# Kernel tuning notes

Measured on AMD Instinct MI355X. Metric: run time of the kernel, lower is better.

## Reference

```python
import jax, jax.numpy as jnp
import numpy as np

B, N, HID = 1, 2048, 2048
NH, NKV, HD = 16, 4, 128
GROUPS = NH // NKV
CHUNK = 64          # get_valid_chunk_size(B*NH*N=32768, 64) == 64
MAG = 0.5
GATE_NORM = 16.0


def setup_inputs() -> dict:
    key = jax.random.key(0)
    ks = jax.random.split(key, 5)
    s = 0.02
    return {
        "hidden_states": jax.random.normal(ks[0], (B, N, HID), jnp.float32),
        "Wq": jax.random.normal(ks[1], (NH * HD, HID), jnp.float32) * s,
        "Wk": jax.random.normal(ks[2], (NKV * HD, HID), jnp.float32) * s,
        "Wv": jax.random.normal(ks[3], (NKV * HD, HID), jnp.float32) * s,
        "Wo": jax.random.normal(ks[4], (HID, NH * HD), jnp.float32) * s,
    }


def _delta_rule_chunked(q, k, v, beta, chunk_size):
    """Chunkwise delta-rule linear attention (DeltaNet chunk form).
    q,k,v,beta: [T, d] flattened tokens; returns (o [T,d], final_state [d,d])."""
    T, d = q.shape
    n = T // chunk_size
    qc, kc, vc, bc = (x.reshape(n, chunk_size, d) for x in (q, k, v, beta))
    kb = kc * bc                       # beta-weighted keys
    vb = vc * bc                       # beta-weighted values
    strict = jnp.tril(jnp.ones((chunk_size, chunk_size), bool), -1)
    eye = jnp.eye(chunk_size, dtype=q.dtype)
    # A = I + strictly-lower(k_beta k^T); unit lower triangular -> invert by triangular solve
    A = eye + jnp.where(strict, jnp.einsum('ncd,nkd->nck', kb, kc), 0.0)
    Tinv = jax.vmap(lambda a: jax.scipy.linalg.solve_triangular(a, eye, lower=True))(A)
    w = Tinv @ kb                      # [n, C, d]
    u = Tinv @ vb                      # [n, C, d]
    causal = jnp.tril(jnp.ones((chunk_size, chunk_size), bool))

    def step(S, inp):
        qi, ki, wi, ui = inp           # each [C, d]
        u_i = ui - wi @ S              # correct pseudo-values by inter-chunk state
        attn = jnp.where(causal, qi @ ki.T, 0.0)
        o = qi @ S + attn @ u_i
        return S + ki.T @ u_i, o

    S0 = jnp.zeros((d, d), q.dtype)
    Sf, o = jax.lax.scan(step, S0, (qc, kc, w, u))
    return o.reshape(T, d), Sf


def _forward(hidden_states, Wq, Wk, Wv, Wo):
    q = hidden_states @ Wq.T           # [B, N, NH*HD]
    k = hidden_states @ Wk.T           # [B, N, NKV*HD]
    v = hidden_states @ Wv.T           # [B, N, NKV*HD]
    g = k                              # AdaptiveAvgPool1d(512 -> 512) is identity
    qh = q.reshape(B, N, NH, HD).transpose(0, 2, 1, 3)   # b h n d
    kh = k.reshape(B, N, NKV, HD).transpose(0, 2, 1, 3)
    vh = v.reshape(B, N, NKV, HD).transpose(0, 2, 1, 3)
    gh = g.reshape(B, N, NKV, HD).transpose(0, 2, 1, 3)
    rep = lambda x: jnp.repeat(x, GROUPS, axis=1)        # repeat_kv
    khr, vhr, ghr = rep(kh), rep(vh), rep(gh)

    # linear-attention path: softmax feature maps + logsigmoid gate
    ql = jax.nn.softmax(qh, axis=-1).astype(jnp.float32)
    kl = jax.nn.softmax(khr, axis=-1).astype(jnp.float32)
    gl = (jax.nn.log_sigmoid(ghr) / GATE_NORM).astype(jnp.float32)
    vl = vhr.astype(jnp.float32)
    flat = lambda x: x.reshape(B * NH * N, HD)
    o_lin, _ = _delta_rule_chunked(flat(ql), flat(kl), flat(vl), flat(gl), CHUNK)
    o_lin = o_lin.reshape(B, NH, N, HD).transpose(0, 2, 1, 3).reshape(B, N, NH * HD)
    o_lin = o_lin @ Wo.T

    # base (vanilla causal softmax) attention path
    scores = jnp.einsum('bhnd,bhmd->bhnm', qh, khr) * (HD ** -0.5)
    cmask = jnp.tril(jnp.ones((N, N), bool))
    scores = jnp.where(cmask[None, None], scores, jnp.finfo(scores.dtype).min)
    attn = jax.nn.softmax(scores, axis=-1)
    o_base = jnp.einsum('bhnm,bhmd->bhnd', attn, vhr)
    o_base = o_base.transpose(0, 2, 1, 3).reshape(B, N, NH * HD) @ Wo.T

    return MAG * o_lin + (1.0 - MAG) * o_base


def reference(hidden_states, Wq, Wk, Wv, Wo):
    return _forward(hidden_states, Wq, Wk, Wv, Wo)
```

## Files before the change

kernel.cpp:

```cpp
#include <hip/hip_runtime.h>
#include <hip/hip_bf16.h>

typedef unsigned short u16;
typedef unsigned int u32;
typedef __bf16 bf16x8 __attribute__((ext_vector_type(8)));
typedef float f32x4 __attribute__((ext_vector_type(4)));

#define MFMA16(a,b,c) __builtin_amdgcn_mfma_f32_16x16x32_bf16((a),(b),(c),0,0,0)

__device__ __forceinline__ u16 f2bf(float f){
  u32 u = __builtin_bit_cast(u32, f);
  u32 r = (u + 0x7fffu + ((u >> 16) & 1u)) >> 16;
  return (u16)r;
}
__device__ __forceinline__ float bf2f(u16 h){
  u32 u = ((u32)h) << 16;
  return __builtin_bit_cast(float, u);
}
__device__ __forceinline__ void splitbf(float x, u16& hi, u16& lo){
  hi = f2bf(x);
  lo = f2bf(x - bf2f(hi));
}
__device__ __forceinline__ void gload_lds16(const u16* g, u16* l){
  __builtin_amdgcn_global_load_lds((__attribute__((address_space(1))) void*)(g),
                                   (__attribute__((address_space(3))) void*)(l), 16, 0, 0);
}
__device__ __forceinline__ const u16* selu(const u16* barr, const u16* parr, int i){
  return (i < 128) ? (barr + (size_t)i*16384) : (parr + (size_t)(i-128)*16384);
}
__device__ __forceinline__ const float* self32(const float* barr, const float* parr, int i){
  return (i < 128) ? (barr + (size_t)i*16384) : (parr + (size_t)(i-128)*16384);
}
__device__ __forceinline__ float* slotp(float* p1, float* p2, int s){
  return (s < 381) ? (p1 + (size_t)s*16512) : (p2 + (size_t)(s-381)*16512);
}
__device__ __forceinline__ const float* slotpc(const float* p1, const float* p2, int s){
  return (s < 381) ? (p1 + (size_t)s*16512) : (p2 + (size_t)(s-381)*16512);
}
__device__ __forceinline__ float* tdq(float* Td, int row, int colc){
  return Td + row*132 + ((colc ^ ((row >> 3) & 7)) << 2);
}

constexpr size_t OF_HSBF   = 0;
constexpr size_t OF_WQKVBF = 8388608;
constexpr size_t OF_WOBF   = 20971520;
constexpr size_t OF_QKV    = 29360128;
constexpr size_t OF_QBF    = 54525952;
constexpr size_t OF_KBF    = 62914560;
constexpr size_t OF_VT     = 65011712;
constexpr size_t OF_QLB    = 67108864;
constexpr size_t OF_KLF    = 75497472;
constexpr size_t OF_KLB    = 79691776;
constexpr size_t OF_GLF    = 81788928;
constexpr size_t OF_TINV   = 85983232;
constexpr size_t OF_WF     = 88080384;
constexpr size_t OF_WB     = 92274688;
constexpr size_t OF_U0     = 94371840;
constexpr size_t OF_SJ     = 111149056;
constexpr size_t OF_OMIX   = 127926272;
constexpr size_t OF_OMIXB  = 144703488;
constexpr size_t OF_ADF  = 102760448;
constexpr size_t OF_ABTF = OF_OMIX;
constexpr size_t OF_ADH  = OF_OMIX + 8388608;
constexpr size_t OF_ADL  = OF_OMIX + 12582912;
constexpr size_t OF_ADTH = OF_OMIXB;
constexpr size_t OF_ADTL = OF_OMIXB + 4194304;
constexpr size_t OF_ABTH = OF_KLF;
constexpr size_t OF_ABTL = OF_GLF;
constexpr size_t OF_BDF  = OF_QKV;
constexpr size_t OF_BBTF = OF_QKV + 8388608;
constexpr size_t OF_BDH  = OF_QKV + 16777216;
constexpr size_t OF_BDL  = OF_QKV + 20971520;
constexpr size_t OF_BDTH = OF_HSBF;
constexpr size_t OF_BDTL = OF_HSBF + 4194304;
constexpr size_t OF_BBTH = OF_WQKVBF;
constexpr size_t OF_BBTL = OF_WQKVBF + 4194304;
constexpr size_t OF_TTF  = OF_TINV;
constexpr size_t OF_TTH  = OF_WQKVBF + 8388608;
constexpr size_t OF_TTL  = OF_WQKVBF + 8912896;
constexpr size_t OF_PDF  = OF_ADF;
constexpr size_t OF_PBTF = OF_ADF + 1048576;
constexpr size_t OF_PDH  = OF_ADF + 2097152;
constexpr size_t OF_PDL  = OF_ADF + 2621440;
constexpr size_t OF_PDTH = OF_ADF + 3145728;
constexpr size_t OF_PDTL = OF_ADF + 3670016;
constexpr size_t OF_PBTH = OF_ADF + 4194304;
constexpr size_t OF_PBTL = OF_ADF + 4718592;
constexpr size_t OF_APART1 = OF_QKV;
constexpr size_t OF_APART2 = OF_OMIXB;
constexpr size_t OF_OBF = 0;

struct CompJobs { int a[8]; int b[8]; int d[8]; };

__global__ void k_f2ball(const float* __restrict__ hs, const float* __restrict__ Wq,
                         const float* __restrict__ Wk, const float* __restrict__ Wv,
                         const float* __restrict__ Wo, u16* __restrict__ hs_bf,
                         u16* __restrict__ wqkv_bf, u16* __restrict__ wo_bf){
  int bid = blockIdx.x;
  const float* src; u16* dst; int off;
  if(bid < 4096){ src = hs; dst = hs_bf; off = bid; }
  else if(bid < 8192){ src = Wq; dst = wqkv_bf; off = bid - 4096; }
  else if(bid < 9216){ src = Wk; dst = wqkv_bf + 2048*2048; off = bid - 8192; }
  else if(bid < 10240){ src = Wv; dst = wqkv_bf + 2560*2048; off = bid - 9216; }
  else { src = Wo; dst = wo_bf; off = bid - 10240; }
  int i = (off*256 + threadIdx.x) * 4;
  f32x4 v = *(const f32x4*)(src + i);
  u32 w0 = (u32)f2bf(v[0]) | ((u32)f2bf(v[1]) << 16);
  u32 w1 = (u32)f2bf(v[2]) | ((u32)f2bf(v[3]) << 16);
  *(u32*)(dst + i) = w0;
  *(u32*)(dst + i + 2) = w1;
}

__global__ __launch_bounds__(256) void k_gemm(const u16* __restrict__ A, const u16* __restrict__ B,
                                              float* __restrict__ C, int K, int N){
  __shared__ u16 aL[128*32];
  __shared__ u16 bL[128*32];
  int lin = blockIdx.y * gridDim.x + blockIdx.x;
  int nwg = gridDim.x * gridDim.y;
  int s = (lin & 7) * (nwg >> 3) + (lin >> 3);
  int bn = s % gridDim.x, bm = s / gridDim.x;
  int tid = threadIdx.x, lane = tid & 63, w = tid >> 6;
  int wm = w >> 1, wn = w & 1;
  f32x4 acc[4][4] = {};
  int nK = K >> 5;
  const u16* Abase = A + (size_t)bm * 128 * K;
  const u16* Bbase = B + (size_t)bn * 128 * K;
  for(int kt = 0; kt < nK; ++kt){
    __syncthreads();
    #pragma unroll
    for(int t = 0; t < 2; ++t){
      int row = t*64 + w*16 + (lane >> 2);
      int kc = (lane & 3) * 8;
      gload_lds16(Abase + (size_t)row*K + kt*32 + kc, &aL[(t*64 + w*16)*32]);
      gload_lds16(Bbase + (size_t)row*K + kt*32 + kc, &bL[(t*64 + w*16)*32]);
    }
    __syncthreads();
    bf16x8 af[4], bf[4];
    #pragma unroll
    for(int i = 0; i < 4; ++i){
      af[i] = *(const bf16x8*)&aL[(wm*64 + i*16 + (lane & 15))*32 + ((lane >> 4) << 3)];
      bf[i] = *(const bf16x8*)&bL[(wn*64 + i*16 + (lane & 15))*32 + ((lane >> 4) << 3)];
    }
    #pragma unroll
    for(int i = 0; i < 4; ++i)
      #pragma unroll
      for(int j = 0; j < 4; ++j)
        acc[i][j] = MFMA16(af[i], bf[j], acc[i][j]);
  }
  #pragma unroll
  for(int i = 0; i < 4; ++i)
    #pragma unroll
    for(int j = 0; j < 4; ++j)
      #pragma unroll
      for(int r = 0; r < 4; ++r){
        int row = bm*128 + wm*64 + i*16 + ((lane >> 4) << 2) + r;
        int col = bn*128 + wn*64 + j*16 + (lane & 15);
        C[(size_t)row * N + col] = acc[i][j][r];
      }
}

__global__ __launch_bounds__(256) void k_linvt(const float* __restrict__ qkv, u16* qbf, u16* qlb,
                                               u16* kbf, float* klf, u16* klb, float* glf,
                                               u16* __restrict__ vT){
  __shared__ float t[64][65];
  int bid = blockIdx.x;
  if(bid < 10240){
    int gtask = bid * 4 + (threadIdx.x >> 6);
    int lane = threadIdx.x & 63;
    int n = gtask / 20, tt = gtask % 20;
    const float* row = (tt < 16) ? (qkv + (size_t)n*3072 + tt*128)
                                 : (qkv + (size_t)n*3072 + 2048 + (tt-16)*128);
    float v0 = row[lane], v1 = row[lane + 64];
    float m = fmaxf(v0, v1);
    #pragma unroll
    for(int o = 1; o < 64; o <<= 1) m = fmaxf(m, __shfl_xor(m, o, 64));
    float e0 = __expf(v0 - m), e1 = __expf(v1 - m);
    float s = e0 + e1;
    #pragma unroll
    for(int o = 1; o < 64; o <<= 1) s += __shfl_xor(s, o, 64);
    float r0 = e0 / s, r1 = e1 / s;
    if(tt < 16){
      size_t base = ((size_t)tt*2048 + n) * 128;
      qbf[base + lane] = f2bf(v0); qbf[base + 64 + lane] = f2bf(v1);
      qlb[base + lane] = f2bf(r0); qlb[base + 64 + lane] = f2bf(r1);
    } else {
      int g = tt - 16;
      size_t base = ((size_t)g*2048 + n) * 128;
      kbf[base + lane] = f2bf(v0); kbf[base + 64 + lane] = f2bf(v1);
      klf[base + lane] = r0;       klf[base + 64 + lane] = r1;
      klb[base + lane] = f2bf(r0); klb[base + 64 + lane] = f2bf(r1);
      float g0 = (fminf(v0, 0.f) - log1pf(__expf(-fabsf(v0)))) * (1.f/16.f);
      float g1 = (fminf(v1, 0.f) - log1pf(__expf(-fabsf(v1)))) * (1.f/16.f);
      glf[base + lane] = g0; glf[base + 64 + lane] = g1;
    }
  } else {
    int v = bid - 10240;
    int nt = v & 31, dt = (v >> 5) & 1, g = v >> 6;
    int tid = threadIdx.x;
    {
      int r = tid >> 2, c0 = (tid & 3) * 16;
      const float* src = qkv + (size_t)(nt*64 + r)*3072 + 2560 + g*128 + dt*64 + c0;
      #pragma unroll
      for(int q = 0; q < 16; q += 4){
        f32x4 vv = *(const f32x4*)(src + q);
        t[r][c0+q] = vv[0]; t[r][c0+q+1] = vv[1]; t[r][c0+q+2] = vv[2]; t[r][c0+q+3] = vv[3];
      }
    }
    __syncthreads();
    {
      int d = tid >> 2, c0 = (tid & 3) * 16;
      u16* dst = vT + ((size_t)g*128 + dt*64 + d)*2048 + (size_t)nt*64 + c0;
      #pragma unroll
      for(int half = 0; half < 2; ++half){
        int b = c0 + half*8;
        u32 w0 = (u32)f2bf(t[b+0][d]) | ((u32)f2bf(t[b+1][d]) << 16);
        u32 w1 = (u32)f2bf(t[b+2][d]) | ((u32)f2bf(t[b+3][d]) << 16);
        u32 w2 = (u32)f2bf(t[b+4][d]) | ((u32)f2bf(t[b+5][d]) << 16);
        u32 w3 = (u32)f2bf(t[b+6][d]) | ((u32)f2bf(t[b+7][d]) << 16);
        *(uint4*)(dst + half*8) = make_uint4(w0, w1, w2, w3);
      }
    }
  }
}

__global__ __launch_bounds__(256) void k_prep1(const float* __restrict__ klf, const float* __restrict__ glf,
                                               float* __restrict__ tinv){
  __shared__ float KlT[128][68];
  __shared__ float Kb[64][132];
  __shared__ float Am[64][68];
  __shared__ float XT[64][68];
  int idx = blockIdx.x, g = idx >> 5, c = idx & 31, tid = threadIdx.x;
  size_t base = ((size_t)g*2048 + c*64) * 128;
  {
    int r = tid >> 2, d0 = (tid & 3) * 32;
    #pragma unroll
    for(int dd = 0; dd < 32; dd += 4){
      f32x4 kv = *(const f32x4*)(klf + base + r*128 + d0 + dd);
      f32x4 gv = *(const f32x4*)(glf + base + r*128 + d0 + dd);
      KlT[d0+dd][r] = kv[0]; KlT[d0+dd+1][r] = kv[1]; KlT[d0+dd+2][r] = kv[2]; KlT[d0+dd+3][r] = kv[3];
      f32x4 kb = kv * gv;
      *(f32x4*)&Kb[r][d0+dd] = kb;
    }
  }
  __syncthreads();
  {
    int i = tid >> 2, j0 = (tid & 3) * 16;
    f32x4 s[4] = {};
    for(int d = 0; d < 128; ++d){
      float kb = Kb[i][d];
      #pragma unroll
      for(int q = 0; q < 4; ++q){
        f32x4 kl = *(const f32x4*)&KlT[d][j0 + q*4];
        s[q] += kb * kl;
      }
    }
    #pragma unroll
    for(int q = 0; q < 4; ++q) *(f32x4*)&Am[i][j0 + q*4] = s[q];
  }
  __syncthreads();
  if(tid < 64){
    int cc = tid;
    float x0 = (cc == 0) ? 1.f : 0.f;
    XT[cc][0] = x0;
    tinv[(size_t)idx*4096 + cc] = x0;
    for(int i = 1; i < 64; ++i){
      float s = (i == cc) ? 1.f : 0.f;
      int i4 = i & ~3;
      for(int jj = 0; jj < i4; jj += 4){
        f32x4 av = *(const f32x4*)&Am[i][jj];
        f32x4 xv = *(const f32x4*)&XT[cc][jj];
        s -= av[0]*xv[0] + av[1]*xv[1] + av[2]*xv[2] + av[3]*xv[3];
      }
      for(int jj = i4; jj < i; ++jj) s -= Am[i][jj] * XT[cc][jj];
      XT[cc][i] = s;
      tinv[(size_t)idx*4096 + i*64 + cc] = s;
    }
  }
}

__global__ __launch_bounds__(256) void k_prep2a(const float* __restrict__ klf, const float* __restrict__ glf,
                                                const float* __restrict__ qkv, const float* __restrict__ tinv,
                                                float* __restrict__ wf, u16* __restrict__ wb, float* __restrict__ u0f){
  __shared__ char smem[51200];
  float (*Ti)[68] = (float(*)[68])smem;
  float (*B)[132] = (float(*)[132])(smem + 17408);
  int bid = blockIdx.x, idx = bid >> 1, z = bid & 1;
  int g = idx >> 5, c = idx & 31, tid = threadIdx.x;
  size_t base = ((size_t)g*2048 + c*64) * 128;
  {
    int r = tid >> 2, d0 = (tid & 3) * 32;
    #pragma unroll
    for(int dd = 0; dd < 32; dd += 4){
      f32x4 gv = *(const f32x4*)(glf + base + r*128 + d0 + dd);
      f32x4 xv;
      if(z == 0) xv = *(const f32x4*)(klf + base + r*128 + d0 + dd);
      else       xv = *(const f32x4*)(qkv + (size_t)(c*64 + r)*3072 + 2560 + g*128 + d0 + dd);
      *(f32x4*)&B[r][d0+dd] = xv * gv;
    }
    int c0 = (tid & 3) * 16;
    #pragma unroll
    for(int q = 0; q < 16; q += 4)
      *(f32x4*)&Ti[r][c0+q] = *(const f32x4*)(tinv + (size_t)idx*4096 + r*64 + c0 + q);
  }
  __syncthreads();
  int i = tid >> 2, cc0 = (tid & 3) * 32;
  f32x4 wa[8] = {};
  for(int jj = 0; jj < 64; ++jj){
    float a = Ti[i][jj];
    #pragma unroll
    for(int q = 0; q < 8; ++q)
      wa[q] += a * *(const f32x4*)&B[jj][cc0 + q*4];
  }
  __syncthreads();
  float (*Tw)[132] = (float(*)[132])smem;
  #pragma unroll
  for(int q = 0; q < 8; ++q)
    *(f32x4*)&Tw[i][cc0 + q*4] = wa[q];
  __syncthreads();
  size_t ob = (size_t)idx * 8192;
  #pragma unroll
  for(int c2 = 0; c2 < 8; ++c2){
    int ii = c2*1024 + tid*4;
    int row = ii >> 7, col = ii & 127;
    f32x4 wv = *(const f32x4*)&Tw[row][col];
    if(z == 0){
      *(f32x4*)(wf + ob + ii) = wv;
      u32 p0 = (u32)f2bf(wv[0]) | ((u32)f2bf(wv[1]) << 16);
      u32 p1 = (u32)f2bf(wv[2]) | ((u32)f2bf(wv[3]) << 16);
      *(u32*)(wb + ob + ii) = p0;
      *(u32*)(wb + ob + ii + 2) = p1;
    } else {
      *(f32x4*)(u0f + ob + ii) = wv;
    }
  }
}

__global__ __launch_bounds__(256) void k_prep2b(const float* __restrict__ klf, const float* __restrict__ wf,
                                                const float* __restrict__ u0f,
                                                float* __restrict__ dF, u16* __restrict__ dH, u16* __restrict__ dL,
                                                u16* __restrict__ dTH, u16* __restrict__ dTL,
                                                float* __restrict__ btF, u16* __restrict__ btH, u16* __restrict__ btL){
  __shared__ char smem[67584];
  float (*Kl)[132] = (float(*)[132])smem;
  float (*Wm)[132] = (float(*)[132])(smem + 33792);
  int bid = blockIdx.x, idx = bid >> 1, z = bid & 1;
  int g = idx >> 5, c = idx & 31, tid = threadIdx.x;
  size_t base = ((size_t)g*2048 + c*64) * 128;
  {
    int r = tid >> 2, d0 = (tid & 3) * 32;
    const float* src = (z == 0) ? wf : u0f;
    #pragma unroll
    for(int dd = 0; dd < 32; dd += 4){
      *(f32x4*)&Kl[r][d0+dd] = *(const f32x4*)(klf + base + r*128 + d0 + dd);
      *(f32x4*)&Wm[r][d0+dd] = *(const f32x4*)(src + (size_t)idx*8192 + r*128 + d0 + dd);
    }
  }
  __syncthreads();
  int a = tid >> 1, b0 = (tid & 1) * 64;
  f32x4 pa[16] = {};
  if(z == 0){
    for(int r = 0; r < 64; ++r){
      float ka = Kl[r][a];
      #pragma unroll
      for(int q = 0; q < 16; ++q)
        pa[q] += ka * *(const f32x4*)&Wm[r][b0 + q*4];
    }
    #pragma unroll
    for(int q = 0; q < 16; ++q) pa[q] = -pa[q];
  } else {
    for(int r = 0; r < 64; ++r){
      float ua = Wm[r][a];
      #pragma unroll
      for(int q = 0; q < 16; ++q)
        pa[q] += ua * *(const f32x4*)&Kl[r][b0 + q*4];
    }
  }
  __syncthreads();
  float* Td = (float*)smem;
  #pragma unroll
  for(int q = 0; q < 16; ++q)
    *(f32x4*)tdq(Td, a, (b0 >> 2) + q) = pa[q];
  __syncthreads();
  size_t ob = (size_t)idx * 16384;
  if(z == 0){
    #pragma unroll
    for(int c2 = 0; c2 < 16; ++c2){
      int ii = c2*1024 + tid*4;
      int row = ii >> 7, col = ii & 127;
      f32x4 dv = *(const f32x4*)tdq(Td, row, col >> 2);
      *(f32x4*)(dF + ob + ii) = dv;
      u16 h0,l0,h1,l1,h2,l2,h3,l3;
      splitbf(dv[0], h0, l0); splitbf(dv[1], h1, l1);
      splitbf(dv[2], h2, l2); splitbf(dv[3], h3, l3);
      *(u32*)(dH + ob + ii)     = (u32)h0 | ((u32)h1 << 16);
      *(u32*)(dH + ob + ii + 2) = (u32)h2 | ((u32)h3 << 16);
      *(u32*)(dL + ob + ii)     = (u32)l0 | ((u32)l1 << 16);
      *(u32*)(dL + ob + ii + 2) = (u32)l2 | ((u32)l3 << 16);
    }
    #pragma unroll
    for(int c2 = 0; c2 < 8; ++c2){
      int o0 = c2*2048 + tid*8;
      int b = o0 >> 7, a0 = o0 & 127;
      u16 th[8], tl[8];
      #pragma unroll
      for(int e = 0; e < 8; ++e){
        float v = *((const float*)tdq(Td, a0 + e, b >> 2) + (b & 3));
        splitbf(v, th[e], tl[e]);
      }
      uint4 ph = make_uint4((u32)th[0] | ((u32)th[1] << 16), (u32)th[2] | ((u32)th[3] << 16),
                            (u32)th[4] | ((u32)th[5] << 16), (u32)th[6] | ((u32)th[7] << 16));
      uint4 plv = make_uint4((u32)tl[0] | ((u32)tl[1] << 16), (u32)tl[2] | ((u32)tl[3] << 16),
                             (u32)tl[4] | ((u32)tl[5] << 16), (u32)tl[6] | ((u32)tl[7] << 16));
      *(uint4*)(dTH + ob + o0) = ph;
      *(uint4*)(dTL + ob + o0) = plv;
    }
  } else {
    #pragma unroll
    for(int c2 = 0; c2 < 16; ++c2){
      int ii = c2*1024 + tid*4;
      int row = ii >> 7, col = ii & 127;
      f32x4 cv = *(const f32x4*)tdq(Td, row, col >> 2);
      *(f32x4*)(btF + ob + ii) = cv;
      u16 h0,l0,h1,l1,h2,l2,h3,l3;
      splitbf(cv[0], h0, l0); splitbf(cv[1], h1, l1);
      splitbf(cv[2], h2, l2); splitbf(cv[3], h3, l3);
      *(u32*)(btH + ob + ii)     = (u32)h0 | ((u32)h1 << 16);
      *(u32*)(btH + ob + ii + 2) = (u32)h2 | ((u32)h3 << 16);
      *(u32*)(btL + ob + ii)     = (u32)l0 | ((u32)l1 << 16);
      *(u32*)(btL + ob + ii + 2) = (u32)l2 | ((u32)l3 << 16);
    }
  }
}

__global__ __launch_bounds__(256) void k_ks(
    const float* __restrict__ sDF, const u16* __restrict__ sDH, const u16* __restrict__ sDL,
    const u16* __restrict__ sDTH, const u16* __restrict__ sDTL,
    const float* __restrict__ sBF, const u16* __restrict__ sBH, const u16* __restrict__ sBL,
    float* __restrict__ dDF, u16* __restrict__ dDH, u16* __restrict__ dDL,
    u16* __restrict__ dDTH, u16* __restrict__ dDTL,
    float* __restrict__ dBF, u16* __restrict__ dBH, u16* __restrict__ dBL, int off){
  __shared__ float T[128][132];
  int c = blockIdx.x, g = blockIdx.y, z = blockIdx.z;
  int idx = g*32 + c, tid = threadIdx.x;
  size_t base = (size_t)idx * 16384;
  if(c < off){
    if(z == 0){
      for(int i = tid; i < 4096; i += 256) ((uint4*)(dDF + base))[i] = ((const uint4*)(sDF + base))[i];
      for(int i = tid; i < 2048; i += 256){
        ((uint4*)(dDH + base))[i] = ((const uint4*)(sDH + base))[i];
        ((uint4*)(dDL + base))[i] = ((const uint4*)(sDL + base))[i];
        ((uint4*)(dDTH + base))[i] = ((const uint4*)(sDTH + base))[i];
        ((uint4*)(dDTL + base))[i] = ((const uint4*)(sDTL + base))[i];
      }
    } else {
      for(int i = tid; i < 4096; i += 256) ((uint4*)(dBF + base))[i] = ((const uint4*)(sBF + base))[i];
      for(int i = tid; i < 2048; i += 256){
        ((uint4*)(dBH + base))[i] = ((const uint4*)(sBH + base))[i];
        ((uint4*)(dBL + base))[i] = ((const uint4*)(sBL + base))[i];
      }
    }
    return;
  }
  size_t blo = (size_t)(idx - off) * 16384;
  int lane = tid & 63, w = tid >> 6;
  const u16 *Ah, *Al, *Bh, *Bl;
  if(z == 0){ Ah = sDH + base; Al = sDL + base; Bh = sDTH + blo; Bl = sDTL + blo; }
  else      { Ah = sBH + blo;  Al = sBL + blo;  Bh = sDH + base; Bl = sDL + base; }
  f32x4 acc[2][8] = {};
  #pragma unroll
  for(int ks = 0; ks < 4; ++ks){
    bf16x8 ah[2], al[2], bh[8], bl[8];
    #pragma unroll
    for(int mt = 0; mt < 2; ++mt){
      int ro = (w*32 + mt*16 + (lane & 15))*128 + ks*32 + ((lane >> 4) << 3);
      ah[mt] = *(const bf16x8*)(Ah + ro);
      al[mt] = *(const bf16x8*)(Al + ro);
    }
    #pragma unroll
    for(int nt = 0; nt < 8; ++nt){
      int ro = (nt*16 + (lane & 15))*128 + ks*32 + ((lane >> 4) << 3);
      bh[nt] = *(const bf16x8*)(Bh + ro);
      bl[nt] = *(const bf16x8*)(Bl + ro);
    }
    #pragma unroll
    for(int mt = 0; mt < 2; ++mt)
      #pragma unroll
      for(int nt = 0; nt < 8; ++nt)
        acc[mt][nt] = MFMA16(ah[mt], bh[nt],
                      MFMA16(ah[mt], bl[nt],
                      MFMA16(al[mt], bh[nt], acc[mt][nt])));
  }
  if(z == 0){
    #pragma unroll
    for(int mt = 0; mt < 2; ++mt)
      #pragma unroll
      for(int nt = 0; nt < 8; ++nt)
        #pragma unroll
        for(int r = 0; r < 4; ++r){
          int row = w*32 + mt*16 + ((lane >> 4) << 2) + r;
          int col = nt*16 + (lane & 15);
          float v = acc[mt][nt][r] + sDF[base + row*128 + col] + sDF[blo + row*128 + col];
          dDF[base + row*128 + col] = v;
          u16 hi, lo; splitbf(v, hi, lo);
          dDH[base + row*128 + col] = hi;
          dDL[base + row*128 + col] = lo;
          T[row][col] = v;
        }
    __syncthreads();
    int tcol = tid >> 1, half = tid & 1;
    for(int m = 0; m < 64; ++m){
      float v = T[half*64 + m][tcol];
      u16 hi, lo; splitbf(v, hi, lo);
      dDTH[base + (size_t)tcol*128 + half*64 + m] = hi;
      dDTL[base + (size_t)tcol*128 + half*64 + m] = lo;
    }
  } else {
    #pragma unroll
    for(int mt = 0; mt < 2; ++mt)
      #pragma unroll
      for(int nt = 0; nt < 8; ++nt)
        #pragma unroll
        for(int r = 0; r < 4; ++r){
          int row = w*32 + mt*16 + ((lane >> 4) << 2) + r;
          int col = nt*16 + (lane & 15);
          float v = acc[mt][nt][r] + sBF[base + row*128 + col] + sBF[blo + row*128 + col];
          dBF[base + row*128 + col] = v;
          u16 hi, lo; splitbf(v, hi, lo);
          dBH[base + row*128 + col] = hi;
          dBL[base + row*128 + col] = lo;
        }
  }
}

__device__ __forceinline__ void comp_mfma(const u16* Ah, const u16* Al, const u16* Bh, const u16* Bl,
                                          f32x4 (&acc)[2][8], int lane, int w){
  #pragma unroll
  for(int ks = 0; ks < 4; ++ks){
    bf16x8 ah[2], al[2], bh[8], bl[8];
    #pragma unroll
    for(int mt = 0; mt < 2; ++mt){
      int ro = (w*32 + mt*16 + (lane & 15))*128 + ks*32 + ((lane >> 4) << 3);
      ah[mt] = *(const bf16x8*)(Ah + ro);
      al[mt] = *(const bf16x8*)(Al + ro);
    }
    #pragma unroll
    for(int nt = 0; nt < 8; ++nt){
      int ro = (nt*16 + (lane & 15))*128 + ks*32 + ((lane >> 4) << 3);
      bh[nt] = *(const bf16x8*)(Bh + ro);
      bl[nt] = *(const bf16x8*)(Bl + ro);
    }
    #pragma unroll
    for(int mt = 0; mt < 2; ++mt)
      #pragma unroll
      for(int nt = 0; nt < 8; ++nt)
        acc[mt][nt] = MFMA16(ah[mt], bh[nt],
                      MFMA16(ah[mt], bl[nt],
                      MFMA16(al[mt], bh[nt], acc[mt][nt])));
  }
}

__global__ __launch_bounds__(256) void k_comp(
    const float* __restrict__ bDF, const u16* __restrict__ bDH, const u16* __restrict__ bDL,
    const u16* __restrict__ bDTH, const u16* __restrict__ bDTL,
    const float* __restrict__ bBTF, const u16* __restrict__ bBTH, const u16* __restrict__ bBTL,
    float* __restrict__ pDF, u16* __restrict__ pDH, u16* __restrict__ pDL,
    u16* __restrict__ pDTH, u16* __restrict__ pDTL,
    float* __restrict__ pBTF, u16* __restrict__ pBTH, u16* __restrict__ pBTL,
    CompJobs jobs){
  __shared__ float T[128][132];
  int job = blockIdx.x, z = blockIdx.y, tid = threadIdx.x;
  int a = jobs.a[job], b = jobs.b[job], d = jobs.d[job] - 128;
  size_t ob = (size_t)d * 16384;
  int lane = tid & 63, w = tid >> 6;
  const u16 *Ah, *Al, *Bh, *Bl;
  const float *F1, *F2;
  if(z == 0){
    Ah = selu(bDH, pDH, a);  Al = selu(bDL, pDL, a);
    Bh = selu(bDTH, pDTH, b); Bl = selu(bDTL, pDTL, b);
    F1 = self32(bDF, pDF, a); F2 = self32(bDF, pDF, b);
  } else {
    Ah = selu(bBTH, pBTH, b); Al = selu(bBTL, pBTL, b);
    Bh = selu(bDH, pDH, a);   Bl = selu(bDL, pDL, a);
    F1 = self32(bBTF, pBTF, a); F2 = self32(bBTF, pBTF, b);
  }
  for(int i = tid*4; i < 16384; i += 1024){
    f32x4 v1 = *(const f32x4*)(F1 + i);
    f32x4 v2 = *(const f32x4*)(F2 + i);
    f32x4 sv = v1 + v2;
    int row = i >> 7, col = i & 127;
    *(f32x4*)&T[row][col] = sv;
  }
  __syncthreads();
  f32x4 acc[2][8] = {};
  comp_mfma(Ah, Al, Bh, Bl, acc, lane, w);
  if(z == 0){
    #pragma unroll
    for(int mt = 0; mt < 2; ++mt)
      #pragma unroll
      for(int nt = 0; nt < 8; ++nt)
        #pragma unroll
        for(int r = 0; r < 4; ++r){
          int row = w*32 + mt*16 + ((lane >> 4) << 2) + r;
          int col = nt*16 + (lane & 15);
          float v = acc[mt][nt][r] + T[row][col];
          pDF[ob + row*128 + col] = v;
          u16 hi, lo; splitbf(v, hi, lo);
          pDH[ob + row*128 + col] = hi;
          pDL[ob + row*128 + col] = lo;
          T[row][col] = v;
        }
    __syncthreads();
    int tcol = tid >> 1, half = tid & 1;
    for(int m = 0; m < 64; ++m){
      float v = T[half*64 + m][tcol];
      u16 hi, lo; splitbf(v, hi, lo);
      pDTH[ob + (size_t)tcol*128 + half*64 + m] = hi;
      pDTL[ob + (size_t)tcol*128 + half*64 + m] = lo;
    }
  } else {
    #pragma unroll
    for(int mt = 0; mt < 2; ++mt)
      #pragma unroll
      for(int nt = 0; nt < 8; ++nt)
        #pragma unroll
        for(int r = 0; r < 4; ++r){
          int row = w*32 + mt*16 + ((lane >> 4) << 2) + r;
          int col = nt*16 + (lane & 15);
          float v = acc[mt][nt][r] + T[row][col];
          pBTF[ob + row*128 + col] = v;
          u16 hi, lo; splitbf(v, hi, lo);
          pBTH[ob + row*128 + col] = hi;
          pBTL[ob + row*128 + col] = lo;
        }
  }
}

__global__ __launch_bounds__(256) void k_heads(
    const u16* __restrict__ bDH, const u16* __restrict__ bDL,
    const float* __restrict__ bBTF, const u16* __restrict__ bBTH, const u16* __restrict__ bBTL,
    const u16* __restrict__ pDH, const u16* __restrict__ pDL,
    const float* __restrict__ pBTF, const u16* __restrict__ pBTH, const u16* __restrict__ pBTL,
    float* __restrict__ ttF, u16* __restrict__ ttH, u16* __restrict__ ttL, u16* __restrict__ sj){
  __shared__ float T[128][132];
  int h = blockIdx.x, g = h >> 2, i0 = h & 3;
  int tid = threadIdx.x, lane = tid & 63, w = tid >> 6;
  int psi = (g == 0) ? -1 : (g == 1 ? 136 : (g == 2 ? 140 : 142));
  int phi = (i0 == 0) ? -1 : (i0 == 1 ? g*32 + 31 : (i0 == 2 ? 128 + g : 132 + g));
  const float* Pf = (psi >= 0) ? self32(bBTF, pBTF, psi) : nullptr;
  const float* Ff = (phi >= 0) ? self32(bBTF, pBTF, phi) : nullptr;
  for(int i = tid*4; i < 16384; i += 1024){
    f32x4 sv = {};
    if(Pf) sv += *(const f32x4*)(Pf + i);
    if(Ff) sv += *(const f32x4*)(Ff + i);
    int row = i >> 7, col = i & 127;
    *(f32x4*)&T[row][col] = sv;
  }
  __syncthreads();
  f32x4 acc[2][8] = {};
  if(psi >= 0 && phi >= 0)
    comp_mfma(selu(bBTH,pBTH,psi), selu(bBTL,pBTL,psi), selu(bDH,pDH,phi), selu(bDL,pDL,phi), acc, lane, w);
  #pragma unroll
  for(int mt = 0; mt < 2; ++mt)
    #pragma unroll
    for(int nt = 0; nt < 8; ++nt)
      #pragma unroll
      for(int r = 0; r < 4; ++r){
        int row = w*32 + mt*16 + ((lane >> 4) << 2) + r;
        int col = nt*16 + (lane & 15);
        float v = acc[mt][nt][r] + T[row][col];
        u16 hi, lo; splitbf(v, hi, lo);
        size_t o = (size_t)h*16384 + row*128 + col;
        ttF[o] = v; ttH[o] = hi; ttL[o] = lo;
        sj[(size_t)(h*32)*16384 + row*128 + col] = hi;
      }
}

__global__ __launch_bounds__(256) void k_expand(const u16* __restrict__ bDH, const u16* __restrict__ bDL,
                                                const float* __restrict__ bBF, const float* __restrict__ ttF,
                                                const u16* __restrict__ ttH, const u16* __restrict__ ttL,
                                                u16* __restrict__ sj){
  int j = blockIdx.x;
  int c = j & 31;
  if(c == 0) return;
  int h = j >> 5, g = h >> 2;
  size_t obase = (size_t)j * 16384;
  size_t mb = (size_t)(g*32 + c - 1) * 16384;
  size_t tb = (size_t)h * 16384;
  int tid = threadIdx.x, lane = tid & 63, w = tid >> 6;
  f32x4 acc[2][8] = {};
  comp_mfma(ttH + tb, ttL + tb, bDH + mb, bDL + mb, acc, lane, w);
  #pragma unroll
  for(int mt = 0; mt < 2; ++mt)
    #pragma unroll
    for(int nt = 0; nt < 8; ++nt)
      #pragma unroll
      for(int r = 0; r < 4; ++r){
        int row = w*32 + mt*16 + ((lane >> 4) << 2) + r;
        int col = nt*16 + (lane & 15);
        float v = acc[mt][nt][r] + ttF[tb + row*128 + col] + bBF[mb + row*128 + col];
        sj[obase + row*128 + col] = f2bf(v);
      }
}

__global__ __launch_bounds__(256) void k_olin(const u16* __restrict__ qlb, const u16* __restrict__ klb,
                                              const u16* __restrict__ wb, const float* __restrict__ u0f,
                                              const u16* __restrict__ sj, float* __restrict__ omix){
  __shared__ u16 ut[128*64];
  __shared__ u16 pl[4][16*64];
  int j = blockIdx.x;
  int h = j >> 5, c = j & 31, g = h >> 2, idx = g*32 + c;
  int tid = threadIdx.x, lane = tid & 63, w = tid >> 6;
  const u16* Sj = sj + (size_t)j * 16384;
  const u16* Q  = qlb + ((size_t)h*2048 + c*64) * 128;
  const u16* Kc = klb + ((size_t)g*2048 + c*64) * 128;
  const u16* W  = wb + (size_t)idx * 8192;
  const float* U0 = u0f + (size_t)idx * 8192;
  bf16x8 aq[4], aw[4];
  #pragma unroll
  for(int ks = 0; ks < 4; ++ks){
    aq[ks] = *(const bf16x8*)(Q + (w*16 + (lane & 15))*128 + ks*32 + ((lane >> 4) << 3));
    aw[ks] = *(const bf16x8*)(W + (w*16 + (lane & 15))*128 + ks*32 + ((lane >> 4) << 3));
  }
  f32x4 t1[8] = {}, ui[8] = {};
  #pragma unroll
  for(int ks = 0; ks < 4; ++ks)
    #pragma unroll
    for(int nt = 0; nt < 8; ++nt){
      bf16x8 b = *(const bf16x8*)(Sj + (nt*16 + (lane & 15))*128 + ks*32 + ((lane >> 4) << 3));
      t1[nt] = MFMA16(aq[ks], b, t1[nt]);
      ui[nt] = MFMA16(aw[ks], b, ui[nt]);
    }
  f32x4 sc[4] = {};
  #pragma unroll
  for(int ks = 0; ks < 4; ++ks)
    #pragma unroll
    for(int nt = 0; nt < 4; ++nt){
      bf16x8 b = *(const bf16x8*)(Kc + (nt*16 + (lane & 15))*128 + ks*32 + ((lane >> 4) << 3));
      sc[nt] = MFMA16(aq[ks], b, sc[nt]);
    }
  #pragma unroll
  for(int nt = 0; nt < 4; ++nt)
    #pragma unroll
    for(int r = 0; r < 4; ++r){
      int row = ((lane >> 4) << 2) + r;
      int col = nt*16 + (lane & 15);
      int grow = w*16 + row;
      float v = (col <= grow) ? sc[nt][r] : 0.f;
      int bo = (row*128 + col*2) ^ ((row & 7) << 4);
      *(u16*)((char*)&pl[w][0] + bo) = f2bf(v);
    }
  #pragma unroll
  for(int nt = 0; nt < 8; ++nt)
    #pragma unroll
    for(int r = 0; r < 4; ++r){
      int kv = w*16 + ((lane >> 4) << 2) + r;
      int d  = nt*16 + (lane & 15);
      float v = U0[kv*128 + d] - ui[nt][r];
      int bo = (d*128 + kv*2) ^ ((d & 7) << 4);
      *(u16*)((char*)ut + bo) = f2bf(v);
    }
  __syncthreads();
  f32x4 o2[8] = {};
  #pragma unroll
  for(int ks2 = 0; ks2 < 2; ++ks2){
    int row = lane & 15;
    int boA = (row*128 + ks2*64 + ((lane >> 4) << 4)) ^ ((row & 7) << 4);
    bf16x8 a = *(const bf16x8*)((const char*)&pl[w][0] + boA);
    #pragma unroll
    for(int nt = 0; nt < 8; ++nt){
      int d = nt*16 + (lane & 15);
      int boB = (d*128 + ks2*64 + ((lane >> 4) << 4)) ^ ((d & 7) << 4);
      bf16x8 b = *(const bf16x8*)((const char*)ut + boB);
      o2[nt] = MFMA16(a, b, o2[nt]);
    }
  }
  #pragma unroll
  for(int nt = 0; nt < 8; ++nt)
    #pragma unroll
    for(int r = 0; r < 4; ++r){
      int grow = c*64 + w*16 + ((lane >> 4) << 2) + r;
      int d = nt*16 + (lane & 15);
      omix[(size_t)grow*2048 + h*128 + d] = 0.5f * (t1[nt][r] + o2[nt][r]);
    }
}

__global__ __launch_bounds__(256) void k_attn(const u16* __restrict__ qbf, const u16* __restrict__ kbf,
                                              const u16* __restrict__ vT, const float* __restrict__ omix,
                                              u16* __restrict__ obf,
                                              float* __restrict__ part1, float* __restrict__ part2){
  __shared__ u16 Kl[4096];
  __shared__ u16 Vl[4096];
  __shared__ u16 pl[4][1280];
  int rb = blockIdx.x;
  int bid = (rb & 7) * 80 + (rb >> 3);
  int h = bid / 40, j = bid % 40;
  int qB, kt0, kt1, slot = -1;
  if(j < 4){ qB = j; kt0 = 0; kt1 = 4*(qB+1); }
  else {
    int jj = j - 4; int seg;
    if(jj < 8){ qB = 4 + (jj >> 1); seg = jj & 1; }
    else if(jj < 20){ int q = jj - 8; qB = 8 + q/3; seg = q - (qB-8)*3; }
    else { int q = jj - 20; qB = 12 + (q >> 2); seg = q & 3; }
    slot = h*36 + jj;
    kt0 = seg*16;
    int full = 4*(qB+1);
    kt1 = (kt0 + 16 < full) ? kt0 + 16 : full;
  }
  int g = h >> 2;
  int tid = threadIdx.x, lane = tid & 63, w = tid >> 6;
  const u16* K = kbf + (size_t)g*2048*128;
  const u16* V = vT + (size_t)g*128*2048;
  bf16x8 aq[2][4];
  #pragma unroll
  for(int m = 0; m < 2; ++m){
    const u16* Q = qbf + ((size_t)h*2048 + qB*128 + w*32 + m*16) * 128;
    #pragma unroll
    for(int ks = 0; ks < 4; ++ks)
      aq[m][ks] = *(const bf16x8*)(Q + (lane & 15)*128 + ks*32 + ((lane >> 4) << 3));
  }
  f32x4 acc[2][8] = {};
  float lsum[2][4] = {};
  const float scale = 0.08838834764831845f;
  int qr0[2];
  #pragma unroll
  for(int m = 0; m < 2; ++m) qr0[m] = qB*128 + w*32 + m*16 + ((lane >> 4) << 2);
  u16* plw = &pl[w][0];
  for(int kt = kt0; kt < kt1; ++kt){
    __syncthreads();
    #pragma unroll
    for(int inst = 0; inst < 2; ++inst){
      int ob = w*2048 + inst*1024;
      int lo = ob + lane*16;
      {
        int r = lo >> 8;
        int gc = ((lo >> 4) & 15) ^ (r & 7);
        gload_lds16(K + (size_t)(kt*32 + r)*128 + gc*8, (u16*)((char*)Kl + ob));
      }
      {
        int d = lo >> 6;
        int gnb = ((lo >> 4) & 3) ^ ((d >> 1) & 3);
        gload_lds16(V + (size_t)d*2048 + kt*32 + gnb*8, (u16*)((char*)Vl + ob));
      }
    }
    __syncthreads();
    bf16x8 kb[8];
    #pragma unroll
    for(int ct = 0; ct < 2; ++ct)
      #pragma unroll
      for(int ks = 0; ks < 4; ++ks){
        int r = ct*16 + (lane & 15);
        int pc = (ks*4 + (lane >> 4)) ^ (r & 7);
        kb[ct*4+ks] = *(const bf16x8*)(Kl + r*128 + pc*8);
      }
    f32x4 s[2][2] = {};
    #pragma unroll
    for(int m = 0; m < 2; ++m)
      #pragma unroll
      for(int ct = 0; ct < 2; ++ct)
        #pragma unroll
        for(int ks = 0; ks < 4; ++ks)
          s[m][ct] = MFMA16(aq[m][ks], kb[ct*4+ks], s[m][ct]);
    bf16x8 bv[8];
    #pragma unroll
    for(int nt = 0; nt < 8; ++nt){
      int d = nt*16 + (lane & 15);
      int pnb = (lane >> 4) ^ ((d >> 1) & 3);
      bv[nt] = *(const bf16x8*)(Vl + d*32 + pnb*8);
    }
    #pragma unroll
    for(int m = 0; m < 2; ++m)
      #pragma unroll
      for(int ct = 0; ct < 2; ++ct)
        #pragma unroll
        for(int r = 0; r < 4; ++r){
          int col = kt*32 + ct*16 + (lane & 15);
          float p = (col <= qr0[m] + r) ? __expf(s[m][ct][r] * scale) : 0.f;
          lsum[m][r] += p;
          int row = m*16 + ((lane >> 4) << 2) + r;
          *(u16*)((char*)plw + row*80 + (ct*16 + (lane & 15))*2) = f2bf(p);
        }
    __builtin_amdgcn_s_setprio(1);
    #pragma unroll
    for(int m = 0; m < 2; ++m){
      bf16x8 ap = *(const bf16x8*)((const char*)plw + (m*16 + (lane & 15))*80 + ((lane >> 4) << 4));
      #pragma unroll
      for(int nt = 0; nt < 8; ++nt)
        acc[m][nt] = MFMA16(ap, bv[nt], acc[m][nt]);
    }
    __builtin_amdgcn_s_setprio(0);
  }
  #pragma unroll
  for(int m = 0; m < 2; ++m)
    #pragma unroll
    for(int r = 0; r < 4; ++r){
      float v = lsum[m][r];
      v += __shfl_xor(v, 1, 64); v += __shfl_xor(v, 2, 64);
      v += __shfl_xor(v, 4, 64); v += __shfl_xor(v, 8, 64);
      lsum[m][r] = v;
    }
  if(slot < 0){
    #pragma unroll
    for(int m = 0; m < 2; ++m)
      #pragma unroll
      for(int nt = 0; nt < 8; ++nt)
        #pragma unroll
        for(int r = 0; r < 4; ++r){
          int row = qB*128 + w*32 + m*16 + ((lane >> 4) << 2) + r;
          int d = nt*16 + (lane & 15);
          size_t o = (size_t)row*2048 + h*128 + d;
          float fin = omix[o] + 0.5f * acc[m][nt][r] / lsum[m][r];
          obf[o] = f2bf(fin);
        }
  } else {
    float* P = slotp(part1, part2, slot);
    #pragma unroll
    for(int m = 0; m < 2; ++m)
      #pragma unroll
      for(int nt = 0; nt < 8; ++nt)
        #pragma unroll
        for(int r = 0; r < 4; ++r){
          int row = w*32 + m*16 + ((lane >> 4) << 2) + r;
          int d = nt*16 + (lane & 15);
          P[(size_t)row*128 + d] = acc[m][nt][r];
        }
    if((lane & 15) == 0)
      #pragma unroll
      for(int m = 0; m < 2; ++m)
        #pragma unroll
        for(int r = 0; r < 4; ++r)
          P[16384 + w*32 + m*16 + ((lane >> 4) << 2) + r] = lsum[m][r];
  }
}

__global__ __launch_bounds__(256) void k_acomb(const float* __restrict__ part1, const float* __restrict__ part2,
                                               const float* __restrict__ omix, u16* __restrict__ obf){
  int bid = blockIdx.x;
  int h = bid / 12, qx = bid % 12, qB = 4 + qx;
  int nseg = (qB >= 12) ? 4 : (qB >= 8) ? 3 : 2;
  int off = (qB < 8) ? (qB-4)*2 : (qB < 12) ? 8 + (qB-8)*3 : 20 + (qB-12)*4;
  int s0 = h*36 + off;
  int tid = threadIdx.x;
  #pragma unroll
  for(int it = 0; it < 16; ++it){
    int i = it*1024 + tid*4;
    int row = i >> 7;
    f32x4 a = {};
    float l = 0.f;
    for(int s = 0; s < nseg; ++s){
      const float* P = slotpc(part1, part2, s0 + s);
      a += *(const f32x4*)(P + i);
      l += P[16384 + row];
    }
    size_t idx = (size_t)(qB*128 + row)*2048 + h*128 + (i & 127);
    f32x4 cur = *(const f32x4*)(omix + idx);
    f32x4 fin = cur + a * (0.5f / l);
    u32 w0 = (u32)f2bf(fin[0]) | ((u32)f2bf(fin[1]) << 16);
    u32 w1 = (u32)f2bf(fin[2]) | ((u32)f2bf(fin[3]) << 16);
    *(u32*)(obf + idx) = w0;
    *(u32*)(obf + idx + 2) = w1;
  }
}

extern "C" void kernel_launch(void* const* d_in, const int* in_sizes, int n_in,
                              void* d_out, int out_size, void* d_ws, size_t ws_size,
                              hipStream_t stream){
  (void)in_sizes; (void)n_in; (void)out_size; (void)ws_size;
  const float* hs = (const float*)d_in[0];
  const float* Wq = (const float*)d_in[1];
  const float* Wk = (const float*)d_in[2];
  const float* Wv = (const float*)d_in[3];
  const float* Wo = (const float*)d_in[4];
  float* out = (float*)d_out;
  char* ws = (char*)d_ws;

  u16*   hs_bf   = (u16*)(ws + OF_HSBF);
  u16*   wqkv_bf = (u16*)(ws + OF_WQKVBF);
  u16*   wo_bf   = (u16*)(ws + OF_WOBF);
  float* qkv     = (float*)(ws + OF_QKV);
  u16*   qbf     = (u16*)(ws + OF_QBF);
  u16*   kbf     = (u16*)(ws + OF_KBF);
  u16*   vT      = (u16*)(ws + OF_VT);
  u16*   qlb     = (u16*)(ws + OF_QLB);
  float* klf     = (float*)(ws + OF_KLF);
  u16*   klb     = (u16*)(ws + OF_KLB);
  float* glf     = (float*)(ws + OF_GLF);
  float* tinvb   = (float*)(ws + OF_TINV);
  float* wf      = (float*)(ws + OF_WF);
  u16*   wb      = (u16*)(ws + OF_WB);
  float* u0f     = (float*)(ws + OF_U0);
  u16*   sjb     = (u16*)(ws + OF_SJ);
  float* omix    = (float*)(ws + OF_OMIX);
  u16*   obf     = (u16*)(ws + OF_OBF);
  float* aDF  = (float*)(ws + OF_ADF);
  u16*   aDH  = (u16*)(ws + OF_ADH);
  u16*   aDL  = (u16*)(ws + OF_ADL);
  u16*   aDTH = (u16*)(ws + OF_ADTH);
  u16*   aDTL = (u16*)(ws + OF_ADTL);
  float* aBTF = (float*)(ws + OF_ABTF);
  u16*   aBTH = (u16*)(ws + OF_ABTH);
  u16*   aBTL = (u16*)(ws + OF_ABTL);
  float* bDF  = (float*)(ws + OF_BDF);
  u16*   bDH  = (u16*)(ws + OF_BDH);
  u16*   bDL  = (u16*)(ws + OF_BDL);
  u16*   bDTH = (u16*)(ws + OF_BDTH);
  u16*   bDTL = (u16*)(ws + OF_BDTL);
  float* bBTF = (float*)(ws + OF_BBTF);
  u16*   bBTH = (u16*)(ws + OF_BBTH);
  u16*   bBTL = (u16*)(ws + OF_BBTL);
  float* ttF  = (float*)(ws + OF_TTF);
  u16*   ttH  = (u16*)(ws + OF_TTH);
  u16*   ttL  = (u16*)(ws + OF_TTL);
  float* pDF  = (float*)(ws + OF_PDF);
  float* pBTF = (float*)(ws + OF_PBTF);
  u16*   pDH  = (u16*)(ws + OF_PDH);
  u16*   pDL  = (u16*)(ws + OF_PDL);
  u16*   pDTH = (u16*)(ws + OF_PDTH);
  u16*   pDTL = (u16*)(ws + OF_PDTL);
  u16*   pBTH = (u16*)(ws + OF_PBTH);
  u16*   pBTL = (u16*)(ws + OF_PBTL);
  float* apart1 = (float*)(ws + OF_APART1);
  float* apart2 = (float*)(ws + OF_APART2);

  k_f2ball<<<14336, 256, 0, stream>>>(hs, Wq, Wk, Wv, Wo, hs_bf, wqkv_bf, wo_bf);
  k_gemm<<<dim3(24, 16), 256, 0, stream>>>(hs_bf, wqkv_bf, qkv, 2048, 3072);
  k_linvt<<<10496, 256, 0, stream>>>(qkv, qbf, qlb, kbf, klf, klb, glf, vT);

  k_prep1<<<128, 256, 0, stream>>>(klf, glf, tinvb);
  k_prep2a<<<256, 256, 0, stream>>>(klf, glf, qkv, tinvb, wf, wb, u0f);
  k_prep2b<<<256, 256, 0, stream>>>(klf, wf, u0f, aDF, aDH, aDL, aDTH, aDTL, aBTF, aBTH, aBTL);

  k_ks<<<dim3(32, 4, 2), 256, 0, stream>>>(aDF, aDH, aDL, aDTH, aDTL, aBTF, aBTH, aBTL,
                                           bDF, bDH, bDL, bDTH, bDTL, bBTF, bBTH, bBTL, 1);
  k_ks<<<dim3(32, 4, 2), 256, 0, stream>>>(bDF, bDH, bDL, bDTH, bDTL, bBTF, bBTH, bBTL,
                                           aDF, aDH, aDL, aDTH, aDTL, aBTF, aBTH, aBTL, 2);
  k_ks<<<dim3(32, 4, 2), 256, 0, stream>>>(aDF, aDH, aDL, aDTH, aDTL, aBTF, aBTH, aBTL,
                                           bDF, bDH, bDL, bDTH, bDTL, bBTF, bBTH, bBTL, 4);
  k_ks<<<dim3(32, 4, 2), 256, 0, stream>>>(bDF, bDH, bDL, bDTH, bDTL, bBTF, bBTH, bBTL,
                                           aDF, aDH, aDL, aDTH, aDTL, aBTF, aBTH, aBTL, 8);
  k_ks<<<dim3(32, 4, 2), 256, 0, stream>>>(aDF, aDH, aDL, aDTH, aDTL, aBTF, aBTH, aBTL,
                                           bDF, bDH, bDL, bDTH, bDTL, bBTF, bBTH, bBTL, 16);

  CompJobs j1{};
  for(int g = 0; g < 4; ++g){ j1.a[g] = g*32+31; j1.b[g] = g*32+31; j1.d[g] = 128+g; }
  k_comp<<<dim3(4, 2), 256, 0, stream>>>(bDF, bDH, bDL, bDTH, bDTL, bBTF, bBTH, bBTL,
                                         pDF, pDH, pDL, pDTH, pDTL, pBTF, pBTH, pBTL, j1);
  CompJobs j2{};
  for(int g = 0; g < 4; ++g){
    j2.a[g]   = 128+g; j2.b[g]   = g*32+31; j2.d[g]   = 132+g;
    j2.a[4+g] = 128+g; j2.b[4+g] = 128+g;   j2.d[4+g] = 136+g;
  }
  k_comp<<<dim3(8, 2), 256, 0, stream>>>(bDF, bDH, bDL, bDTH, bDTL, bBTF, bBTH, bBTL,
                                         pDF, pDH, pDL, pDTH, pDTL, pBTF, pBTH, pBTL, j2);
  CompJobs j3{};
  j3.a[0] = 137; j3.b[0] = 136; j3.d[0] = 140;
  j3.a[1] = 138; j3.b[1] = 137; j3.d[1] = 141;
  k_comp<<<dim3(2, 2), 256, 0, stream>>>(bDF, bDH, bDL, bDTH, bDTL, bBTF, bBTH, bBTL,
                                         pDF, pDH, pDL, pDTH, pDTL, pBTF, pBTH, pBTL, j3);
  CompJobs j4{};
  j4.a[0] = 141; j4.b[0] = 136; j4.d[0] = 142;
  k_comp<<<dim3(1, 2), 256, 0, stream>>>(bDF, bDH, bDL, bDTH, bDTL, bBTF, bBTH, bBTL,
                                         pDF, pDH, pDL, pDTH, pDTL, pBTF, pBTH, pBTL, j4);

  k_heads<<<16, 256, 0, stream>>>(bDH, bDL, bBTF, bBTH, bBTL,
                                  pDH, pDL, pBTF, pBTH, pBTL, ttF, ttH, ttL, sjb);
  k_expand<<<512, 256, 0, stream>>>(bDH, bDL, bBTF, ttF, ttH, ttL, sjb);

  k_olin<<<512, 256, 0, stream>>>(qlb, klb, wb, u0f, sjb, omix);
  k_attn<<<640, 256, 0, stream>>>(qbf, kbf, vT, omix, obf, apart1, apart2);
  k_acomb<<<192, 256, 0, stream>>>(apart1, apart2, omix, obf);

  k_gemm<<<dim3(16, 16), 256, 0, stream>>>(obf, wo_bf, out, 2048, 2048);
}
```

Before: 617.4 us.

## Split-K the QKV and output projection GEMMs with partial-sum combine

```diff
diff --git a/kernel.cpp b/kernel.cpp
--- a/kernel.cpp
+++ b/kernel.cpp
@@ -89,6 +89,9 @@
 constexpr size_t OF_APART1 = OF_QKV;
 constexpr size_t OF_APART2 = OF_OMIXB;
 constexpr size_t OF_OBF = 0;
+constexpr size_t OF_QKVB  = OF_SJ;
+constexpr size_t OF_OUTH0 = OF_QKV;
+constexpr size_t OF_OUTH1 = OF_QKV + 16777216;
 
 struct CompJobs { int a[8]; int b[8]; int d[8]; };
 
@@ -112,19 +115,25 @@
 }
 
 __global__ __launch_bounds__(256) void k_gemm(const u16* __restrict__ A, const u16* __restrict__ B,
-                                              float* __restrict__ C, int K, int N){
+                                              float* __restrict__ C0, float* __restrict__ C1,
+                                              int K, int N){
   __shared__ u16 aL[128*32];
   __shared__ u16 bL[128*32];
-  int lin = blockIdx.y * gridDim.x + blockIdx.x;
-  int nwg = gridDim.x * gridDim.y;
+  int nxy = gridDim.x * gridDim.y;
+  int nwg = nxy * gridDim.z;
+  int lin = (blockIdx.z * gridDim.y + blockIdx.y) * gridDim.x + blockIdx.x;
   int s = (lin & 7) * (nwg >> 3) + (lin >> 3);
-  int bn = s % gridDim.x, bm = s / gridDim.x;
+  int z = s / nxy; int rem = s - z * nxy;
+  int bn = rem % gridDim.x, bm = rem / gridDim.x;
+  float* C = (z == 0) ? C0 : C1;
+  int kspan = K / gridDim.z;
+  int k0 = z * kspan;
   int tid = threadIdx.x, lane = tid & 63, w = tid >> 6;
   int wm = w >> 1, wn = w & 1;
   f32x4 acc[4][4] = {};
-  int nK = K >> 5;
-  const u16* Abase = A + (size_t)bm * 128 * K;
-  const u16* Bbase = B + (size_t)bn * 128 * K;
+  int nK = kspan >> 5;
+  const u16* Abase = A + (size_t)bm * 128 * K + k0;
+  const u16* Bbase = B + (size_t)bn * 128 * K + k0;
   for(int kt = 0; kt < nK; ++kt){
     __syncthreads();
     #pragma unroll
@@ -159,7 +168,16 @@
       }
 }
 
-__global__ __launch_bounds__(256) void k_linvt(const float* __restrict__ qkv, u16* qbf, u16* qlb,
+__global__ void k_ocomb(const float* __restrict__ h0, const float* __restrict__ h1,
+                        float* __restrict__ out){
+  int i = (blockIdx.x * 256 + threadIdx.x) * 4;
+  f32x4 a = *(const f32x4*)(h0 + i);
+  f32x4 b = *(const f32x4*)(h1 + i);
+  *(f32x4*)(out + i) = a + b;
+}
+
+__global__ __launch_bounds__(256) void k_linvt(float* __restrict__ qkv, const float* __restrict__ qkvB,
+                                               u16* qbf, u16* qlb,
                                                u16* kbf, float* klf, u16* klb, float* glf,
                                                u16* __restrict__ vT){
   __shared__ float t[64][65];
@@ -168,9 +186,12 @@
     int gtask = bid * 4 + (threadIdx.x >> 6);
     int lane = threadIdx.x & 63;
     int n = gtask / 20, tt = gtask % 20;
-    const float* row = (tt < 16) ? (qkv + (size_t)n*3072 + tt*128)
-                                 : (qkv + (size_t)n*3072 + 2048 + (tt-16)*128);
-    float v0 = row[lane], v1 = row[lane + 64];
+    size_t ro = (tt < 16) ? ((size_t)n*3072 + tt*128)
+                          : ((size_t)n*3072 + 2048 + (tt-16)*128);
+    const float* rowA = qkv + ro;
+    const float* rowB = qkvB + ro;
+    float v0 = rowA[lane] + rowB[lane];
+    float v1 = rowA[lane + 64] + rowB[lane + 64];
     float m = fmaxf(v0, v1);
     #pragma unroll
     for(int o = 1; o < 64; o <<= 1) m = fmaxf(m, __shfl_xor(m, o, 64));
@@ -199,10 +220,13 @@
     int tid = threadIdx.x;
     {
       int r = tid >> 2, c0 = (tid & 3) * 16;
-      const float* src = qkv + (size_t)(nt*64 + r)*3072 + 2560 + g*128 + dt*64 + c0;
+      size_t so = (size_t)(nt*64 + r)*3072 + 2560 + g*128 + dt*64 + c0;
+      float* srcA = qkv + so;
+      const float* srcB = qkvB + so;
       #pragma unroll
       for(int q = 0; q < 16; q += 4){
-        f32x4 vv = *(const f32x4*)(src + q);
+        f32x4 vv = *(const f32x4*)(srcA + q) + *(const f32x4*)(srcB + q);
+        *(f32x4*)(srcA + q) = vv;
         t[r][c0+q] = vv[0]; t[r][c0+q+1] = vv[1]; t[r][c0+q+2] = vv[2]; t[r][c0+q+3] = vv[3];
       }
     }
@@ -977,6 +1001,7 @@
   u16*   wqkv_bf = (u16*)(ws + OF_WQKVBF);
   u16*   wo_bf   = (u16*)(ws + OF_WOBF);
   float* qkv     = (float*)(ws + OF_QKV);
+  float* qkvB    = (float*)(ws + OF_QKVB);
   u16*   qbf     = (u16*)(ws + OF_QBF);
   u16*   kbf     = (u16*)(ws + OF_KBF);
   u16*   vT      = (u16*)(ws + OF_VT);
@@ -991,6 +1016,8 @@
   u16*   sjb     = (u16*)(ws + OF_SJ);
   float* omix    = (float*)(ws + OF_OMIX);
   u16*   obf     = (u16*)(ws + OF_OBF);
+  float* outh0   = (float*)(ws + OF_OUTH0);
+  float* outh1   = (float*)(ws + OF_OUTH1);
   float* aDF  = (float*)(ws + OF_ADF);
   u16*   aDH  = (u16*)(ws + OF_ADH);
   u16*   aDL  = (u16*)(ws + OF_ADL);
@@ -1022,8 +1049,8 @@
   float* apart2 = (float*)(ws + OF_APART2);
 
   k_f2ball<<<14336, 256, 0, stream>>>(hs, Wq, Wk, Wv, Wo, hs_bf, wqkv_bf, wo_bf);
-  k_gemm<<<dim3(24, 16), 256, 0, stream>>>(hs_bf, wqkv_bf, qkv, 2048, 3072);
-  k_linvt<<<10496, 256, 0, stream>>>(qkv, qbf, qlb, kbf, klf, klb, glf, vT);
+  k_gemm<<<dim3(24, 16, 2), 256, 0, stream>>>(hs_bf, wqkv_bf, qkv, qkvB, 2048, 3072);
+  k_linvt<<<10496, 256, 0, stream>>>(qkv, qkvB, qbf, qlb, kbf, klf, klb, glf, vT);
 
   k_prep1<<<128, 256, 0, stream>>>(klf, glf, tinvb);
   k_prep2a<<<256, 256, 0, stream>>>(klf, glf, qkv, tinvb, wf, wb, u0f);
@@ -1069,5 +1096,6 @@
   k_attn<<<640, 256, 0, stream>>>(qbf, kbf, vT, omix, obf, apart1, apart2);
   k_acomb<<<192, 256, 0, stream>>>(apart1, apart2, omix, obf);
 
-  k_gemm<<<dim3(16, 16), 256, 0, stream>>>(obf, wo_bf, out, 2048, 2048);
-}
+  k_gemm<<<dim3(16, 16, 2), 256, 0, stream>>>(obf, wo_bf, outh0, outh1, 2048, 2048);
+  k_ocomb<<<4096, 256, 0, stream>>>(outh0, outh1, out);
+}
```

Result: faster. 602.1 us (median of 3 runs) (-2.5%).
